# Performance work log

Measured on AMD Instinct MI355X. Metric: run time of the kernel, lower is better.

## Reference

```python
import jax, jax.numpy as jnp
import numpy as np
import math

N_LAYERS = 2; D = 768; D_INNER = 1536; N = 16; DR = 48; K = 4
VOCAB = 32000; B = 2; L = 1024
EPS = 1e-5


def setup_inputs() -> dict:
    key = jax.random.key(0)
    k = jax.random.split(key, 10)
    x = jax.random.randint(k[0], (B, L), 0, VOCAB)
    embedding = jax.random.normal(k[1], (VOCAB, D), jnp.float32) * 0.02
    rms_w = jnp.ones((N_LAYERS, D), jnp.float32)
    in_proj_w = jax.random.normal(k[2], (N_LAYERS, 2 * D_INNER, D), jnp.float32) * 0.02
    conv_w = jax.random.normal(k[3], (N_LAYERS, D_INNER, K), jnp.float32) * 0.1
    conv_b = jnp.zeros((N_LAYERS, D_INNER), jnp.float32)
    # S4D-real init: A[d, n] = n+1, stored as log(-A) = log(A)
    A0 = jnp.log(jnp.broadcast_to(jnp.arange(1, N + 1, dtype=jnp.float32), (D_INNER, N)))
    log_minus_A = jnp.tile(A0[None], (N_LAYERS, 1, 1))
    bcdelta_w = jax.random.normal(k[4], (N_LAYERS, 2 * N + DR, D_INNER), jnp.float32) * 0.02
    s = DR ** -0.5  # delta_init='random', delta_scale=1.0
    dup_w = jax.random.uniform(k[5], (N_LAYERS, D_INNER, DR), jnp.float32, minval=-s, maxval=s)
    u = jax.random.uniform(k[6], (N_LAYERS, D_INNER), jnp.float32)
    samp = jnp.maximum(jnp.exp((math.log(0.1) - math.log(0.001)) * u + math.log(0.001)), 1e-4)
    dup_b = samp + jnp.log(-jnp.expm1(-samp))  # softplus-inverse
    D_param = jnp.ones((N_LAYERS, D_INNER), jnp.float32)
    out_proj_w = jax.random.normal(k[7], (N_LAYERS, D, D_INNER), jnp.float32) * (0.02 / math.sqrt(N_LAYERS))
    norm_f_w = jnp.ones((D,), jnp.float32)
    return dict(x=x, embedding=embedding, rms_w=rms_w, in_proj_w=in_proj_w,
                conv_w=conv_w, conv_b=conv_b, log_minus_A=log_minus_A,
                bcdelta_w=bcdelta_w, dup_w=dup_w, dup_b=dup_b,
                D_param=D_param, out_proj_w=out_proj_w, norm_f_w=norm_f_w)


def _rmsnorm(h, w):
    return h * jax.lax.rsqrt(jnp.mean(h * h, axis=-1, keepdims=True) + EPS) * w


def _causal_conv(h, w, b):
    # depthwise causal conv: torch Conv1d(pad=K-1)[..., :L]
    hp = jnp.pad(h, ((0, 0), (K - 1, 0), (0, 0)))  # (b, l+K-1, d)
    Lh = h.shape[1]
    y = sum(hp[:, k:k + Lh, :] * w[:, k] for k in range(K))
    return y + b


def _s6(h, lA, bcw, dw, db, Dp):
    bcd = h @ bcw.T                                    # (b, l, 2N+DR)
    Bm, Cm, dlt = jnp.split(bcd, [N, 2 * N], axis=-1)
    delta = jax.nn.softplus(dlt @ dw.T + db)           # (b, l, d)
    A = -jnp.exp(lA)                                   # (d, n), negative
    dA = jnp.einsum('bld,dn->bldn', delta, A)
    A_bar = jnp.exp(dA)
    B_bar = (A_bar - 1.0) / dA * jnp.einsum('bld,bln->bldn', delta, Bm)
    u = B_bar * h[..., None]                           # (b, l, d, n)

    def step(hs, inp):
        a, ui, c = inp
        hs = a * hs + ui                               # (b, d, n)
        return hs, jnp.einsum('bn,bdn->bd', c, hs)

    h0 = jnp.zeros((h.shape[0], h.shape[2], N), h.dtype)
    _, ys = jax.lax.scan(step, h0, (jnp.swapaxes(A_bar, 0, 1),
                                    jnp.swapaxes(u, 0, 1),
                                    jnp.swapaxes(Cm, 0, 1)))
    return jnp.swapaxes(ys, 0, 1) + h * Dp


def _block(h, in_w, cw, cb, lA, bcw, dw, db, Dp, ow):
    xz = h @ in_w.T
    xi, res = jnp.split(xz, 2, axis=-1)
    xi = jax.nn.silu(_causal_conv(xi, cw, cb))
    y = _s6(xi, lA, bcw, dw, db, Dp)
    return (y * jax.nn.silu(res)) @ ow.T


def reference(x, embedding, rms_w, in_proj_w, conv_w, conv_b, log_minus_A,
              bcdelta_w, dup_w, dup_b, D_param, out_proj_w, norm_f_w):
    h = embedding[x]                                   # (b, l, D)
    for i in range(N_LAYERS):
        h = _block(_rmsnorm(h, rms_w[i]), in_proj_w[i], conv_w[i], conv_b[i],
                   log_minus_A[i], bcdelta_w[i], dup_w[i], dup_b[i],
                   D_param[i], out_proj_w[i]) + h
    h = _rmsnorm(h, norm_f_w)
    return h @ embedding.T                             # tied logits (b, l, V)
```

## Files before the change

### kernel.cpp

```cpp
#include <hip/hip_runtime.h>
#include <math.h>

#define BB 2
#define LL 1024
#define DD 768
#define DI 1536
#define NS 16
#define DRR 48
#define KC 4
#define VOC 32000
#define BT (BB*LL)
#define EPS 1e-5f

#define NCH 16
#define TC  (LL/NCH)
#define CHW ((DI/16)*256)

typedef __attribute__((ext_vector_type(4))) float f32x4;
typedef __attribute__((ext_vector_type(8))) short short8;
typedef unsigned short ushort_t;

__device__ __forceinline__ unsigned short f2bf(float f) {
    unsigned int u = __float_as_uint(f);
    u += 0x7FFFu + ((u >> 16) & 1u);
    return (unsigned short)(u >> 16);
}

#define GLDS(gp, lp) __builtin_amdgcn_global_load_lds( \
    (const __attribute__((address_space(1))) unsigned int*)(gp), \
    (__attribute__((address_space(3))) unsigned int*)(lp), 16, 0, 0)

#define DPP_ADD(c, ctrl) ((c) + __int_as_float(__builtin_amdgcn_update_dpp( \
    0, __float_as_int(c), (ctrl), 0xF, 0xF, true)))

template<bool ADD, bool NMASK, bool ATOMIC>
__global__ __launch_bounds__(256) void gemm_bf16(
    const ushort_t* __restrict__ A, const ushort_t* __restrict__ W,
    float* C, int Nn, int lda, int ldc, int kchunk)
{
    __shared__ __align__(16) ushort_t As[128 * 32];
    __shared__ __align__(16) ushort_t Ws[128 * 32];

    const int row0 = blockIdx.x * 128;
    const int col0 = blockIdx.y * 128;
    const int tid  = threadIdx.x;
    const int lane = tid & 63;
    const int wave = tid >> 6;
    const int wm   = (wave & 1) * 64;
    const int wn   = (wave >> 1) * 64;
    const int mrow = lane & 15;
    const int quad = lane >> 4;

    const int kb = blockIdx.z * kchunk;

    const int srow = tid >> 2;
    const int scol = (tid & 3) << 3;
    const ushort_t* gA0 = A + (size_t)(row0 + srow) * lda + scol;
    const ushort_t* gA1 = A + (size_t)(row0 + 64 + srow) * lda + scol;
    const ushort_t* gW0 = W + (size_t)(col0 + srow) * lda + scol;
    const ushort_t* gW1 = W + (size_t)(col0 + 64 + srow) * lda + scol;
    char* lA0 = (char*)As + wave * 1024;
    char* lA1 = (char*)As + 4096 + wave * 1024;
    char* lW0 = (char*)Ws + wave * 1024;
    char* lW1 = (char*)Ws + 4096 + wave * 1024;

    f32x4 acc[4][4];
#pragma unroll
    for (int i = 0; i < 4; ++i)
#pragma unroll
        for (int j = 0; j < 4; ++j)
            acc[i][j] = (f32x4){0.f, 0.f, 0.f, 0.f};

    for (int k0 = kb; k0 < kb + kchunk; k0 += 32) {
        GLDS(gA0 + k0, lA0);
        GLDS(gA1 + k0, lA1);
        GLDS(gW0 + k0, lW0);
        GLDS(gW1 + k0, lW1);
        __syncthreads();

        short8 af[4], wf[4];
#pragma unroll
        for (int i = 0; i < 4; ++i) {
            af[i] = *(const short8*)&As[(wm + i * 16 + mrow) * 32 + quad * 8];
            wf[i] = *(const short8*)&Ws[(wn + i * 16 + mrow) * 32 + quad * 8];
        }
#pragma unroll
        for (int i = 0; i < 4; ++i)
#pragma unroll
            for (int j = 0; j < 4; ++j)
                acc[i][j] = __builtin_amdgcn_mfma_f32_16x16x32_bf16(
                    af[i], wf[j], acc[i][j], 0, 0, 0);
        __syncthreads();
    }

#pragma unroll
    for (int i = 0; i < 4; ++i)
#pragma unroll
        for (int j = 0; j < 4; ++j)
#pragma unroll
            for (int r = 0; r < 4; ++r) {
                int row = row0 + wm + i * 16 + quad * 4 + r;
                int col = col0 + wn + j * 16 + mrow;
                if (!NMASK || col < Nn) {
                    float v = acc[i][j][r];
                    size_t off = (size_t)row * ldc + col;
                    if (ATOMIC) {
                        atomicAdd(&C[off], v);
                    } else {
                        if (ADD) v += C[off];
                        C[off] = v;
                    }
                }
            }
}

__global__ __launch_bounds__(256) void cvt_bf16_kernel(
    const float* __restrict__ in, ushort_t* __restrict__ out, int n4)
{
    int i = blockIdx.x * 256 + threadIdx.x;
    if (i >= n4) return;
    float4 v = ((const float4*)in)[i];
    ushort4 o;
    o.x = f2bf(v.x); o.y = f2bf(v.y); o.z = f2bf(v.z); o.w = f2bf(v.w);
    ((ushort4*)out)[i] = o;
}

__global__ __launch_bounds__(256) void cvt_bcw_kernel(
    const float* __restrict__ bcw, ushort_t* __restrict__ out)
{
    int i = blockIdx.x * 256 + threadIdx.x;
    if (i >= 2 * 128 * 1536 / 4) return;
    int e = i * 4;
    int layer = e / (128 * 1536);
    int rem = e % (128 * 1536);
    int row = rem / 1536, col = rem % 1536;
    ushort4 o = {0, 0, 0, 0};
    if (row < 80) {
        float4 v = *(const float4*)(bcw + ((size_t)layer * 80 + row) * 1536 + col);
        o.x = f2bf(v.x); o.y = f2bf(v.y); o.z = f2bf(v.z); o.w = f2bf(v.w);
    }
    ((ushort4*)out)[i] = o;
}

__global__ __launch_bounds__(256) void zero_kernel(float* __restrict__ p, int n)
{
    int i = blockIdx.x * 256 + threadIdx.x;
    if (i < n) p[i] = 0.f;
}

__global__ __launch_bounds__(256) void embed_kernel(
    const int* __restrict__ x, const float* __restrict__ emb, float* __restrict__ h)
{
    int idx = blockIdx.x * 256 + threadIdx.x;
    if (idx >= BT * (DD / 4)) return;
    int row = idx / (DD / 4), c = idx % (DD / 4);
    ((float4*)h)[idx] = ((const float4*)(emb + (size_t)x[row] * DD))[c];
}

__global__ __launch_bounds__(256) void rmsnorm_kernel(
    const float* __restrict__ h, const float* __restrict__ w, ushort_t* __restrict__ out)
{
    int row = blockIdx.x, tid = threadIdx.x;
    const float* hr = h + (size_t)row * DD;
    float s = 0.f;
    for (int i = tid; i < DD; i += 256) { float v = hr[i]; s += v * v; }
#pragma unroll
    for (int off = 32; off >= 1; off >>= 1) s += __shfl_xor(s, off);
    __shared__ float part[4];
    if ((tid & 63) == 0) part[tid >> 6] = s;
    __syncthreads();
    float tot = part[0] + part[1] + part[2] + part[3];
    float sc = rsqrtf(tot * (1.0f / DD) + EPS);
    for (int i = tid; i < DD; i += 256)
        out[(size_t)row * DD + i] = f2bf(hr[i] * sc * w[i]);
}

__global__ __launch_bounds__(256) void conv_silu_kernel(
    const float* __restrict__ xz, const float* __restrict__ cw,
    const float* __restrict__ cb, float* __restrict__ xi, ushort_t* __restrict__ xi16)
{
    int idx = blockIdx.x * 256 + threadIdx.x;
    if (idx >= BT * DI) return;
    int d = idx % DI, bt = idx / DI, t = bt % LL;
    const float* base = xz + (size_t)bt * (2 * DI) + d;
    float w0 = cw[d * 4 + 0], w1 = cw[d * 4 + 1], w2 = cw[d * 4 + 2], w3 = cw[d * 4 + 3];
    float acc = cb[d] + base[0] * w3;
    if (t >= 1) acc += base[-(ptrdiff_t)(2 * DI)] * w2;
    if (t >= 2) acc += base[-(ptrdiff_t)(4 * DI)] * w1;
    if (t >= 3) acc += base[-(ptrdiff_t)(6 * DI)] * w0;
    float v = acc / (1.0f + expf(-acc));
    xi[idx] = v;
    xi16[idx] = f2bf(v);
}

__global__ __launch_bounds__(256) void delta_kernel(
    const float* __restrict__ bcd, const float* __restrict__ dw,
    const float* __restrict__ db, float* __restrict__ delta)
{
    int row = blockIdx.x / 6, chunk = blockIdx.x % 6;
    int d = chunk * 256 + threadIdx.x;
    __shared__ float dlt_s[DRR];
    if (threadIdx.x < DRR) dlt_s[threadIdx.x] = bcd[(size_t)row * 80 + 32 + threadIdx.x];
    __syncthreads();
    float z = db[d];
    const float* wr = dw + (size_t)d * DRR;
#pragma unroll
    for (int r = 0; r < DRR; ++r) z = fmaf(dlt_s[r], wr[r], z);
    delta[(size_t)row * DI + d] = (z > 20.f) ? z : log1pf(expf(z));
}

__global__ __launch_bounds__(256) void scan_pass1(
    const float* __restrict__ delta, const float* __restrict__ xi,
    const float* __restrict__ bcd, const float* __restrict__ lA,
    float* __restrict__ a_cum, float* __restrict__ h_end)
{
    int blk  = blockIdx.x;
    int c    = blk % NCH;
    int rest = blk / NCH;
    int b    = rest / (DI / 16);
    int dbi  = rest % (DI / 16);
    int dblk = dbi * 16;
    int tid  = threadIdx.x, lane = tid & 63, wave = tid >> 6;
    int n = lane & 15, dl = wave * 4 + (lane >> 4), d = dblk + dl;

    float Av   = -expf(lA[(size_t)d * NS + n]);
    float A2   = Av * 1.44269504088896f;
    float invA = 1.0f / Av;

    __shared__ float2 s_dx[TC][16];
    __shared__ float  s_B [TC][16];

    const float* dbase = delta + ((size_t)b * LL + c * TC) * DI + dblk;
    const float* xbase = xi    + ((size_t)b * LL + c * TC) * DI + dblk;
    const float* bcb   = bcd   + ((size_t)b * LL + c * TC) * 80;

    for (int i = tid; i < TC * 16; i += 256) {
        int tt = i >> 4, dd = i & 15;
        s_dx[tt][dd] = make_float2(dbase[(size_t)tt * DI + dd],
                                   xbase[(size_t)tt * DI + dd]);
        s_B[tt][dd]  = bcb[(size_t)tt * 80 + dd];
    }
    __syncthreads();

    float hs = 0.f, sd = 0.f;
#pragma unroll 4
    for (int tt = 0; tt < TC; ++tt) {
        float2 dx = s_dx[tt][dl];
        float Bv  = s_B[tt][n];
        float Ab  = exp2f(dx.x * A2);
        float u   = (Ab - 1.0f) * invA * Bv * dx.y;
        hs = fmaf(Ab, hs, u);
        sd += dx.x;
    }
    size_t o = (((size_t)b * NCH + c) * (DI / 16) + dbi) * 256 + dl * 16 + n;
    a_cum[o] = exp2f(A2 * sd);
    h_end[o] = hs;
}

__global__ __launch_bounds__(256) void scan_pass2(
    const float* __restrict__ a_cum, const float* __restrict__ h_end,
    float* __restrict__ h_init)
{
    int gid = blockIdx.x * 256 + threadIdx.x;
    if (gid >= BB * CHW) return;
    int b = gid / CHW, r = gid % CHW;
    size_t base = (size_t)b * NCH * CHW + r;
    float h = 0.f;
#pragma unroll
    for (int c = 0; c < NCH; ++c) {
        h_init[base + (size_t)c * CHW] = h;
        h = fmaf(a_cum[base + (size_t)c * CHW], h, h_end[base + (size_t)c * CHW]);
    }
}

__global__ __launch_bounds__(256) void scan_pass3(
    const float* __restrict__ delta, const float* __restrict__ xi,
    const float* __restrict__ bcd, const float* __restrict__ lA,
    const float* __restrict__ Dp, const float* __restrict__ h_init,
    float* __restrict__ y)
{
    int blk  = blockIdx.x;
    int c    = blk % NCH;
    int rest = blk / NCH;
    int b    = rest / (DI / 16);
    int dbi  = rest % (DI / 16);
    int dblk = dbi * 16;
    int tid  = threadIdx.x, lane = tid & 63, wave = tid >> 6;
    int n = lane & 15, dl = wave * 4 + (lane >> 4), d = dblk + dl;

    float Av   = -expf(lA[(size_t)d * NS + n]);
    float A2   = Av * 1.44269504088896f;
    float invA = 1.0f / Av;
    float Dpv  = Dp[d];

    __shared__ float2 s_dx[TC][16];
    __shared__ float2 s_bc[TC][16];

    const float* dbase = delta + ((size_t)b * LL + c * TC) * DI + dblk;
    const float* xbase = xi    + ((size_t)b * LL + c * TC) * DI + dblk;
    const float* bcb   = bcd   + ((size_t)b * LL + c * TC) * 80;
    float*       ybase = y     + ((size_t)b * LL + c * TC) * DI + dblk;

    for (int i = tid; i < TC * 16; i += 256) {
        int tt = i >> 4, dd = i & 15;
        s_dx[tt][dd] = make_float2(dbase[(size_t)tt * DI + dd],
                                   xbase[(size_t)tt * DI + dd]);
        s_bc[tt][dd] = make_float2(bcb[(size_t)tt * 80 + dd],
                                   bcb[(size_t)tt * 80 + 16 + dd]);
    }
    __syncthreads();

    float hs = h_init[(((size_t)b * NCH + c) * (DI / 16) + dbi) * 256 + dl * 16 + n];

#pragma unroll 4
    for (int tt = 0; tt < TC; ++tt) {
        float2 dx = s_dx[tt][dl];
        float2 bc = s_bc[tt][n];
        float Ab  = exp2f(dx.x * A2);
        float u   = (Ab - 1.0f) * invA * bc.x * dx.y;
        hs = fmaf(Ab, hs, u);
        float r = bc.y * hs;
        r = DPP_ADD(r, 0xB1);
        r = DPP_ADD(r, 0x4E);
        r = DPP_ADD(r, 0x141);
        r = DPP_ADD(r, 0x140);
        if (n == 0) ybase[(size_t)tt * DI + dl] = fmaf(dx.y, Dpv, r);
    }
}

__global__ __launch_bounds__(256) void gate_kernel(
    const float* __restrict__ y, const float* __restrict__ xz, ushort_t* __restrict__ yg16)
{
    int idx = blockIdx.x * 256 + threadIdx.x;
    if (idx >= BT * DI) return;
    int d = idx % DI, bt = idx / DI;
    float r = xz[(size_t)bt * (2 * DI) + DI + d];
    yg16[idx] = f2bf(y[idx] * r / (1.0f + expf(-r)));
}

extern "C" void kernel_launch(void* const* d_in, const int* in_sizes, int n_in,
                              void* d_out, int out_size, void* d_ws, size_t ws_size,
                              hipStream_t stream)
{
    const int*   x    = (const int*)  d_in[0];
    const float* emb  = (const float*)d_in[1];
    const float* rmsw = (const float*)d_in[2];
    const float* inw  = (const float*)d_in[3];
    const float* cw   = (const float*)d_in[4];
    const float* cb   = (const float*)d_in[5];
    const float* lA   = (const float*)d_in[6];
    const float* bcw  = (const float*)d_in[7];
    const float* dw   = (const float*)d_in[8];
    const float* db   = (const float*)d_in[9];
    const float* Dp   = (const float*)d_in[10];
    const float* ow   = (const float*)d_in[11];
    const float* nfw  = (const float*)d_in[12];
    float* out = (float*)d_out;

    float* ws = (float*)d_ws;
    float* h    = ws;
    float* xz   = h    + (size_t)BT * DD;
    float* xi   = xz   + (size_t)BT * 2 * DI;
    float* bcd  = xi   + (size_t)BT * DI;
    float* dlt  = bcd  + (size_t)BT * 80;
    float* yb   = dlt  + (size_t)BT * DI;
    float* acum = yb   + (size_t)BT * DI;
    float* hend = acum + (size_t)BB * NCH * DI * NS;
    float* hini = hend + (size_t)BB * NCH * DI * NS;
    ushort_t* bf = (ushort_t*)(hini + (size_t)BB * NCH * DI * NS);
    ushort_t* hn_bf  = bf;
    ushort_t* xib_bf = hn_bf  + (size_t)BT * DD;
    ushort_t* yg_bf  = xib_bf + (size_t)BT * DI;
    ushort_t* emb_bf = yg_bf  + (size_t)BT * DI;
    ushort_t* inw_bf = emb_bf + (size_t)VOC * DD;
    ushort_t* ow_bf  = inw_bf + (size_t)2 * 2 * DI * DD;
    ushort_t* bcw_bf = ow_bf  + (size_t)2 * DD * DI;

    cvt_bf16_kernel<<<(VOC * DD / 4 + 255) / 256, 256, 0, stream>>>(emb, emb_bf, VOC * DD / 4);
    cvt_bf16_kernel<<<(2 * 2 * DI * DD / 4 + 255) / 256, 256, 0, stream>>>(inw, inw_bf, 2 * 2 * DI * DD / 4);
    cvt_bf16_kernel<<<(2 * DD * DI / 4 + 255) / 256, 256, 0, stream>>>(ow, ow_bf, 2 * DD * DI / 4);
    cvt_bcw_kernel<<<(2 * 128 * 1536 / 4 + 255) / 256, 256, 0, stream>>>(bcw, bcw_bf);

    embed_kernel<<<(BT * (DD / 4) + 255) / 256, 256, 0, stream>>>(x, emb, h);

    for (int layer = 0; layer < 2; ++layer) {
        rmsnorm_kernel<<<BT, 256, 0, stream>>>(h, rmsw + (size_t)layer * DD, hn_bf);

        gemm_bf16<false, false, false><<<dim3(BT / 128, 2 * DI / 128, 1), 256, 0, stream>>>(
            hn_bf, inw_bf + (size_t)layer * 2 * DI * DD, xz, 2 * DI, DD, 2 * DI, DD);

        conv_silu_kernel<<<(BT * DI + 255) / 256, 256, 0, stream>>>(
            xz, cw + (size_t)layer * DI * KC, cb + (size_t)layer * DI, xi, xib_bf);

        zero_kernel<<<(BT * 80 + 255) / 256, 256, 0, stream>>>(bcd, BT * 80);

        gemm_bf16<false, true, true><<<dim3(BT / 128, 1, 8), 256, 0, stream>>>(
            xib_bf, bcw_bf + (size_t)layer * 128 * 1536, bcd, 80, DI, 80, DI / 8);

        delta_kernel<<<BT * 6, 256, 0, stream>>>(
            bcd, dw + (size_t)layer * DI * DRR, db + (size_t)layer * DI, dlt);

        scan_pass1<<<BB * (DI / 16) * NCH, 256, 0, stream>>>(
            dlt, xi, bcd, lA + (size_t)layer * DI * NS, acum, hend);
        scan_pass2<<<(BB * CHW + 255) / 256, 256, 0, stream>>>(acum, hend, hini);
        scan_pass3<<<BB * (DI / 16) * NCH, 256, 0, stream>>>(
            dlt, xi, bcd, lA + (size_t)layer * DI * NS, Dp + (size_t)layer * DI, hini, yb);

        gate_kernel<<<(BT * DI + 255) / 256, 256, 0, stream>>>(yb, xz, yg_bf);

        gemm_bf16<true, false, false><<<dim3(BT / 128, DD / 128, 1), 256, 0, stream>>>(
            yg_bf, ow_bf + (size_t)layer * DD * DI, h, DD, DI, DD, DI);
    }

    rmsnorm_kernel<<<BT, 256, 0, stream>>>(h, nfw, hn_bf);

    gemm_bf16<false, false, false><<<dim3(BT / 128, VOC / 128, 1), 256, 0, stream>>>(
        hn_bf, emb_bf, out, VOC, DD, VOC, DD);
}
```

Baseline: 926.0 us.

## Add dedicated 256x256 pipelined bf16 GEMM for tied-embedding logits

Replaces the generic 128x128 GEMM for the final logits projection with a specialized 256x256-tile, 512-thread kernel. It streams global-to-LDS loads several stages ahead, using vmcnt waits and scheduling barriers to overlap loads with MFMA. It also uses an XOR-swizzled LDS layout and remaps block IDs for L2 locality. The logits GEMM is the largest matmul in the model, so this targets most of the runtime. The cost is a 128 KB LDS footprint and hard-coded shapes (K=768, N=32000).

```diff
diff --git a/kernel.cpp b/kernel.cpp
--- a/kernel.cpp
+++ b/kernel.cpp
@@ -112,6 +112,136 @@
                     }
                 }
             }
+}
+
+#define GK  768
+#define GN  32000
+#define NT12 12
+
+__device__ __forceinline__ void stage_unit(
+    int j, char* ldsw, const char* sA0, const char* sA1,
+    const char* sB0, const char* sB1)
+{
+    if (j >= 4 * NT12) return;
+    int tt = j >> 2, hh = (j >> 1) & 1, ee = j & 1;
+    int koff = tt * 128 + hh * 64;
+    char* dst = ldsw + (j & 7) * 16384;
+    const char* s0 = (ee ? sB0 : sA0) + koff;
+    const char* s1 = (ee ? sB1 : sA1) + koff;
+    GLDS(s0, dst);
+    GLDS(s1, dst + 8192);
+}
+
+#define VMCNT(N) asm volatile("s_waitcnt vmcnt(" #N ")" ::: "memory")
+
+#define SBAR() do { __builtin_amdgcn_sched_barrier(0); \
+    __builtin_amdgcn_s_barrier(); \
+    __builtin_amdgcn_sched_barrier(0); } while (0)
+
+#define MFMA16(M2) do { \
+    __builtin_amdgcn_s_setprio(1); \
+    _Pragma("unroll") \
+    for (int i_ = 0; i_ < 4; ++i_) \
+        _Pragma("unroll") \
+        for (int n_ = 0; n_ < 4; ++n_) \
+            acc[(M2)*4 + i_][n_] = __builtin_amdgcn_mfma_f32_16x16x32_bf16( \
+                af[i_], wf[n_], acc[(M2)*4 + i_][n_], 0, 0, 0); \
+    __builtin_amdgcn_s_setprio(0); \
+} while (0)
+
+#define PHASE(T, H, M2, LOADB, WAITSTMT) do { \
+    const char* bufA_ = ldsc + ((T) & 1) * 65536 + (H) * 32768; \
+    if (LOADB) { \
+        _Pragma("unroll") \
+        for (int n_ = 0; n_ < 4; ++n_) \
+            wf[n_] = *(const short8*)(bufA_ + 16384 + offB[n_]); \
+    } \
+    _Pragma("unroll") \
+    for (int i_ = 0; i_ < 4; ++i_) \
+        af[i_] = *(const short8*)(bufA_ + offA[(M2)*4 + i_]); \
+    stage_unit(4*(T) + 2*(H) + (M2) + 6, ldsw, sA0, sA1, sB0, sB1); \
+    SBAR(); \
+    MFMA16(M2); \
+    WAITSTMT; \
+    SBAR(); \
+} while (0)
+
+#define TILE(T, W1, W2) do { \
+    PHASE(T, 0, 0, true,  (void)0); \
+    PHASE(T, 0, 1, false, W1); \
+    PHASE(T, 1, 0, true,  (void)0); \
+    PHASE(T, 1, 1, false, W2); \
+} while (0)
+
+__global__ __launch_bounds__(512, 2) void gemm_logits_256(
+    const ushort_t* __restrict__ A, const ushort_t* __restrict__ W,
+    float* __restrict__ C)
+{
+    __shared__ __align__(16) char ldsc[131072];
+
+    const int bid = blockIdx.x;
+    const int s   = (bid & 7) * 125 + (bid >> 3);
+    const int mt  = s & 7;
+    const int nt  = s >> 3;
+
+    const int tid  = threadIdx.x;
+    const int lane = tid & 63;
+    const int wave = tid >> 6;
+    const int wm   = wave >> 2;
+    const int wn   = wave & 3;
+    const int mrow = lane & 15;
+    const int quad = lane >> 4;
+
+    int offA[8], offB[4];
+#pragma unroll
+    for (int m = 0; m < 8; ++m) {
+        int r = wm * 128 + m * 16 + mrow;
+        offA[m] = r * 64 + ((quad * 16) ^ (((r >> 1) & 3) << 4));
+    }
+#pragma unroll
+    for (int n = 0; n < 4; ++n) {
+        int r = wn * 64 + n * 16 + mrow;
+        offB[n] = r * 64 + ((quad * 16) ^ (((r >> 1) & 3) << 4));
+    }
+
+    const int X0 = tid * 16;
+    const int L0 = X0 ^ (((X0 >> 7) & 3) << 4);
+    const int r0 = L0 >> 6, c0 = L0 & 63;
+    const char* sA0 = (const char*)A + ((size_t)(mt * 256 +       r0) * GK) * 2 + c0;
+    const char* sA1 = (const char*)A + ((size_t)(mt * 256 + 128 + r0) * GK) * 2 + c0;
+    const char* sB0 = (const char*)W + ((size_t)(nt * 256 +       r0) * GK) * 2 + c0;
+    const char* sB1 = (const char*)W + ((size_t)(nt * 256 + 128 + r0) * GK) * 2 + c0;
+    char* ldsw = ldsc + wave * 1024;
+
+    f32x4 acc[8][4];
+#pragma unroll
+    for (int m = 0; m < 8; ++m)
+#pragma unroll
+        for (int n = 0; n < 4; ++n)
+            acc[m][n] = (f32x4){0.f, 0.f, 0.f, 0.f};
+
+    short8 af[4], wf[4];
+
+#pragma unroll
+    for (int j = 0; j < 6; ++j)
+        stage_unit(j, ldsw, sA0, sA1, sB0, sB1);
+    VMCNT(8);
+    SBAR();
+
+    for (int t = 0; t < NT12 - 2; ++t)
+        TILE(t, VMCNT(8), VMCNT(8));
+    TILE(10, VMCNT(8), VMCNT(4));
+    TILE(11, VMCNT(0), (void)0);
+
+    float* Cb = C + (size_t)(mt * 256 + wm * 128 + quad * 4) * GN
+                  + nt * 256 + wn * 64 + mrow;
+#pragma unroll
+    for (int m = 0; m < 8; ++m)
+#pragma unroll
+        for (int r = 0; r < 4; ++r)
+#pragma unroll
+            for (int n = 0; n < 4; ++n)
+                Cb[(size_t)(m * 16 + r) * GN + n * 16] = acc[m][n][r];
 }
 
 __global__ __launch_bounds__(256) void cvt_bf16_kernel(
@@ -414,6 +544,6 @@
 
     rmsnorm_kernel<<<BT, 256, 0, stream>>>(h, nfw, hn_bf);
 
-    gemm_bf16<false, false, false><<<dim3(BT / 128, VOC / 128, 1), 256, 0, stream>>>(
-        hn_bf, emb_bf, out, VOC, DD, VOC, DD);
-}
+    gemm_logits_256<<<dim3(BT / 256 * (VOC / 256)), 512, 0, stream>>>(
+        hn_bf, emb_bf, out);
+}
```

After: 880.4 us. 4.9% less time.
